# Performance work log

Hardware: AMD Instinct MI355X
Metric: run time of the kernel (lower is better)

## Reference

```python
import jax, jax.numpy as jnp
import numpy as np

B, S, DM, H, D = 4, 2048, 1024, 16, 64
CAP = 15.0
EPS = 1e-6


def setup_inputs() -> dict:
    key = jax.random.key(0)
    ks = jax.random.split(key, 5)
    return {
        "x": jax.random.normal(ks[0], (B, S, DM), jnp.float32),
        "hidden_state": jnp.zeros((B, H, D, D), jnp.float32),
        "w_qkv": jax.random.normal(ks[1], (3 * H * D, DM), jnp.float32) * 0.02,
        "w_gate": jax.random.normal(ks[2], (3 * H, DM), jnp.float32) * 0.02,
        "w_out": jax.random.normal(ks[3], (DM, H * D), jnp.float32) * 0.02,
        "ln_w": jnp.ones((DM,), jnp.float32),
    }


def reference(x, hidden_state, w_qkv, w_gate, w_out, ln_w):
    Bq, Sq, DMq = x.shape
    residual = x
    # RMSNorm (computed in float32, matching the torch module)
    xf = x.astype(jnp.float32)
    var = jnp.mean(xf * xf, axis=-1, keepdims=True)
    xn = ln_w * (xf * jax.lax.rsqrt(var + EPS)).astype(x.dtype)
    # Fused qkv projection: (B,S,3,H,D)
    qkv = jnp.einsum('bsd,od->bso', xn, w_qkv).reshape(Bq, Sq, 3, H, D)
    q, k, v = qkv[:, :, 0], qkv[:, :, 1], qkv[:, :, 2]
    # Gates: (B,S,3,H) -> soft cap -> sigmoid
    gates = jnp.einsum('bsd,od->bso', xn, w_gate).reshape(Bq, Sq, 3, H)
    gates = jax.nn.sigmoid(CAP * jnp.tanh(gates / CAP))
    ig, fg, og = gates[:, :, 0], gates[:, :, 1], gates[:, :, 2]

    def step(h, inp):
        q_t, k_t, v_t, i_t, f_t, o_t = inp  # q/k/v: (B,H,D); gates: (B,H)
        kv = jnp.einsum('bhd,bhe->bhde', k_t, v_t)
        h = f_t[..., None, None] * h + i_t[..., None, None] * kv
        out = o_t[..., None] * jnp.einsum('bhd,bhde->bhe', q_t, h)
        return h, out

    xs = (q.swapaxes(0, 1), k.swapaxes(0, 1), v.swapaxes(0, 1),
          ig.swapaxes(0, 1), fg.swapaxes(0, 1), og.swapaxes(0, 1))
    h_final, outs = jax.lax.scan(step, hidden_state, xs)  # outs: (S,B,H,D)
    output = outs.swapaxes(0, 1).reshape(Bq, Sq, H * D)
    y = residual + output @ w_out.T
    return y, h_final
```

## Files before the change

### kernel.cpp

```cpp
#include <hip/hip_runtime.h>
#include <hip/hip_bf16.h>
#include <math.h>
#include <stdint.h>

#define Bq 4
#define Sq 2048
#define DMq 1024
#define Hq 16
#define Dq 64
#define CAPf 15.0f
#define EPSf 1e-6f
#define Tc 64
#define Cc (Sq / Tc)
#define QKVW (3 * Hq * Dq)
#define NGATE (3 * Hq)
#define NMERGE (QKVW + NGATE)
#define NPAD 3200

typedef __attribute__((ext_vector_type(8))) short short8;
typedef __attribute__((ext_vector_type(4))) float f32x4;
typedef __hip_bfloat16 bf16;

__device__ __forceinline__ float b2f(bf16 v) { return __bfloat162float(v); }
__device__ __forceinline__ bf16  f2b(float v) { return __float2bfloat16(v); }
__device__ __forceinline__ uint16_t f2bu(float f) {
    bf16 h = __float2bfloat16(f); uint16_t u; __builtin_memcpy(&u, &h, 2); return u;
}
__device__ __forceinline__ float bu2f(uint16_t u) {
    uint32_t x = ((uint32_t)u) << 16; float f; __builtin_memcpy(&f, &x, 4); return f;
}
__device__ __forceinline__ float gate_act(float v) {
    float t = v * (1.0f / CAPf);
    float e2 = __expf(2.0f * t);
    float th = 1.0f - 2.0f / (e2 + 1.0f);
    return 1.0f / (1.0f + __expf(-CAPf * th));
}

__global__ void convert_all(const float* __restrict__ wqkv,
                            const float* __restrict__ wgate,
                            const float* __restrict__ wout,
                            bf16* __restrict__ wcomb, bf16* __restrict__ wob) {
    const int n1 = QKVW * DMq / 4;
    const int n2 = (NPAD - QKVW) * DMq / 4;
    const int ng = NGATE * DMq / 4;
    const int n3 = DMq * Hq * Dq / 4;
    int i = blockIdx.x * 256 + threadIdx.x;
    if (i < n1) {
        float4 v = ((const float4*)wqkv)[i];
        bf16 t[4] = {f2b(v.x), f2b(v.y), f2b(v.z), f2b(v.w)};
        ((uint2*)wcomb)[i] = *(uint2*)t;
    } else if (i < n1 + n2) {
        int j = i - n1;
        uint2 o = make_uint2(0u, 0u);
        if (j < ng) {
            float4 v = ((const float4*)wgate)[j];
            bf16 t[4] = {f2b(v.x), f2b(v.y), f2b(v.z), f2b(v.w)};
            o = *(uint2*)t;
        }
        ((uint2*)wcomb)[n1 + j] = o;
    } else if (i < n1 + n2 + n3) {
        int j = i - n1 - n2;
        float4 v = ((const float4*)wout)[j];
        bf16 t[4] = {f2b(v.x), f2b(v.y), f2b(v.z), f2b(v.w)};
        ((uint2*)wob)[j] = *(uint2*)t;
    }
}

__global__ void rmsnorm_kernel(const float* __restrict__ x,
                               const float* __restrict__ ln_w,
                               bf16* __restrict__ xn) {
    int row = blockIdx.x;
    const float4* xr = (const float4*)(x + (size_t)row * DMq);
    int tid = threadIdx.x;
    float4 v = xr[tid];
    float ss = v.x*v.x + v.y*v.y + v.z*v.z + v.w*v.w;
    #pragma unroll
    for (int off = 32; off > 0; off >>= 1) ss += __shfl_down(ss, off);
    __shared__ float red[4];
    int lane = tid & 63, wv = tid >> 6;
    if (lane == 0) red[wv] = ss;
    __syncthreads();
    float tot = red[0] + red[1] + red[2] + red[3];
    float rs = rsqrtf(tot * (1.0f / DMq) + EPSf);
    float4 w4 = ((const float4*)ln_w)[tid];
    bf16 t[4] = {f2b(v.x * rs * w4.x), f2b(v.y * rs * w4.y),
                 f2b(v.z * rs * w4.z), f2b(v.w * rs * w4.w)};
    *(uint2*)(xn + (size_t)row * DMq + tid * 4) = *(uint2*)t;
}

__device__ __forceinline__ int2 xcd_swizzle(int gx) {
    int wg = blockIdx.y * gx + blockIdx.x;
    int nwg = gx * gridDim.y;
    int cpx = nwg >> 3;
    int swz = (wg & 7) * cpx + (wg >> 3);
    return make_int2(swz % gx, swz / gx);
}

__global__ __launch_bounds__(256) void gemm_qkvgate(const bf16* __restrict__ A,
                                                    const bf16* __restrict__ Bw,
                                                    bf16* __restrict__ qkvb,
                                                    float* __restrict__ gates,
                                                    int M, int N, int K) {
    __shared__ bf16 As[128 * 64];
    __shared__ bf16 Bs[128 * 64];
    const int tid = threadIdx.x;
    const int w = tid >> 6;
    const int l = tid & 63;
    const int wr = (w >> 1) * 64;
    const int wc = (w & 1) * 64;
    int2 bxy = xcd_swizzle(gridDim.x);
    const int bm = bxy.y * 128;
    const int bn = bxy.x * 128;

    const int lrow = l >> 3;
    const int swzc = ((l & 7) ^ lrow) * 8;
    const int fl = l & 15;
    const int kb = l >> 4;
    const int rsw = l & 7;

    f32x4 acc[4][4];
    #pragma unroll
    for (int i = 0; i < 4; i++)
        #pragma unroll
        for (int j = 0; j < 4; j++) acc[i][j] = (f32x4){0.f, 0.f, 0.f, 0.f};

    for (int k0 = 0; k0 < K; k0 += 64) {
        __syncthreads();
        #pragma unroll
        for (int inst = 0; inst < 4; inst++) {
            int r0 = w * 32 + inst * 8;
            const bf16* gp = A + (size_t)(bm + r0 + lrow) * K + k0 + swzc;
            __builtin_amdgcn_global_load_lds(
                (const __attribute__((address_space(1))) uint32_t*)gp,
                (__attribute__((address_space(3))) uint32_t*)(As + r0 * 64),
                16, 0, 0);
        }
        #pragma unroll
        for (int inst = 0; inst < 4; inst++) {
            int r0 = w * 32 + inst * 8;
            if (bn + r0 < N) {
                const bf16* gp = Bw + (size_t)(bn + r0 + lrow) * K + k0 + swzc;
                __builtin_amdgcn_global_load_lds(
                    (const __attribute__((address_space(1))) uint32_t*)gp,
                    (__attribute__((address_space(3))) uint32_t*)(Bs + r0 * 64),
                    16, 0, 0);
            }
        }
        __syncthreads();
        #pragma unroll
        for (int kk2 = 0; kk2 < 2; kk2++) {
            const int koff = (((kk2 << 2) + kb) ^ rsw) * 8;
            short8 af[4], bfr[4];
            #pragma unroll
            for (int i = 0; i < 4; i++)
                af[i] = *(const short8*)(As + (wr + i * 16 + fl) * 64 + koff);
            #pragma unroll
            for (int j = 0; j < 4; j++)
                bfr[j] = *(const short8*)(Bs + (wc + j * 16 + fl) * 64 + koff);
            #pragma unroll
            for (int i = 0; i < 4; i++)
                #pragma unroll
                for (int j = 0; j < 4; j++)
                    acc[i][j] = __builtin_amdgcn_mfma_f32_16x16x32_bf16(
                        af[i], bfr[j], acc[i][j], 0, 0, 0);
        }
    }

    #pragma unroll
    for (int i = 0; i < 4; i++) {
        #pragma unroll
        for (int j = 0; j < 4; j++) {
            int col = bn + wc + j * 16 + fl;
            #pragma unroll
            for (int r = 0; r < 4; r++) {
                int row = bm + wr + i * 16 + kb * 4 + r;
                float v = acc[i][j][r];
                if (col < QKVW) {
                    qkvb[(size_t)row * QKVW + col] = f2b(v);
                } else if (col < NMERGE) {
                    gates[(size_t)row * NGATE + (col - QKVW)] = v;
                }
            }
        }
    }
}

__global__ __launch_bounds__(256) void gemm_out(const bf16* __restrict__ A,
                                                const bf16* __restrict__ Bw,
                                                const float* __restrict__ resid,
                                                float* __restrict__ C,
                                                int M, int N, int K) {
    __shared__ bf16 As[128 * 64];
    __shared__ bf16 Bs[128 * 64];
    const int tid = threadIdx.x;
    const int w = tid >> 6;
    const int l = tid & 63;
    const int wr = (w >> 1) * 64;
    const int wc = (w & 1) * 64;
    int2 bxy = xcd_swizzle(gridDim.x);
    const int bm = bxy.y * 128;
    const int bn = bxy.x * 128;

    const int lrow = l >> 3;
    const int swzc = ((l & 7) ^ lrow) * 8;
    const int fl = l & 15;
    const int kb = l >> 4;
    const int rsw = l & 7;

    f32x4 acc[4][4];
    #pragma unroll
    for (int i = 0; i < 4; i++)
        #pragma unroll
        for (int j = 0; j < 4; j++) acc[i][j] = (f32x4){0.f, 0.f, 0.f, 0.f};

    for (int k0 = 0; k0 < K; k0 += 64) {
        __syncthreads();
        #pragma unroll
        for (int inst = 0; inst < 4; inst++) {
            int r0 = w * 32 + inst * 8;
            const bf16* gp = A + (size_t)(bm + r0 + lrow) * K + k0 + swzc;
            __builtin_amdgcn_global_load_lds(
                (const __attribute__((address_space(1))) uint32_t*)gp,
                (__attribute__((address_space(3))) uint32_t*)(As + r0 * 64),
                16, 0, 0);
        }
        #pragma unroll
        for (int inst = 0; inst < 4; inst++) {
            int r0 = w * 32 + inst * 8;
            const bf16* gp = Bw + (size_t)(bn + r0 + lrow) * K + k0 + swzc;
            __builtin_amdgcn_global_load_lds(
                (const __attribute__((address_space(1))) uint32_t*)gp,
                (__attribute__((address_space(3))) uint32_t*)(Bs + r0 * 64),
                16, 0, 0);
        }
        __syncthreads();
        #pragma unroll
        for (int kk2 = 0; kk2 < 2; kk2++) {
            const int koff = (((kk2 << 2) + kb) ^ rsw) * 8;
            short8 af[4], bfr[4];
            #pragma unroll
            for (int i = 0; i < 4; i++)
                af[i] = *(const short8*)(As + (wr + i * 16 + fl) * 64 + koff);
            #pragma unroll
            for (int j = 0; j < 4; j++)
                bfr[j] = *(const short8*)(Bs + (wc + j * 16 + fl) * 64 + koff);
            #pragma unroll
            for (int i = 0; i < 4; i++)
                #pragma unroll
                for (int j = 0; j < 4; j++)
                    acc[i][j] = __builtin_amdgcn_mfma_f32_16x16x32_bf16(
                        af[i], bfr[j], acc[i][j], 0, 0, 0);
        }
    }

    #pragma unroll
    for (int i = 0; i < 4; i++) {
        #pragma unroll
        for (int j = 0; j < 4; j++) {
            int col = bn + wc + j * 16 + fl;
            #pragma unroll
            for (int r = 0; r < 4; r++) {
                int row = bm + wr + i * 16 + kb * 4 + r;
                size_t idx = (size_t)row * N + col;
                C[idx] = acc[i][j][r] + resid[idx];
            }
        }
    }
}

__global__ __launch_bounds__(64) void chunk_intra(const bf16* __restrict__ qkvb,
                                                  const float* __restrict__ gates,
                                                  bf16* __restrict__ attb,
                                                  bf16* __restrict__ LT,
                                                  float* __restrict__ oaArr,
                                                  float* __restrict__ Fch) {
    const int blk = blockIdx.x;
    const int c  = blk & (Cc - 1);
    const int bh = blk >> 5;
    const int b = bh >> 4, hh = bh & 15;
    const int l = threadIdx.x;
    const int s0 = c * Tc;

    __shared__ bf16 KTs[4096];
    __shared__ bf16 VTs[4096];
    __shared__ bf16 Ps[4096];
    __shared__ float rowS[64], pcolS[64], wstS[64];

    const float* gp = gates + (size_t)(b * Sq + s0 + l) * NGATE;
    float ig = gate_act(gp[hh]);
    float fg = gate_act(gp[Hq + hh]);
    float og = gate_act(gp[2 * Hq + hh]);
    float la = __logf(fg);
    #pragma unroll
    for (int off = 1; off < 64; off <<= 1) {
        float v = __shfl_up(la, off);
        if (l >= off) la += v;
    }
    float la63 = __shfl(la, 63);
    float li = __logf(ig);
    rowS[l]  = la + __logf(og);
    pcolS[l] = li - la;
    wstS[l]  = __expf(la63 - la + li);
    float oa = og * __expf(la);
    oaArr[(size_t)blk * 64 + l] = oa;
    if (l == 0) Fch[blk] = __expf(la63);
    __syncthreads();

    const int cg = l & 7, rp = l >> 3;
    const size_t rowBase = (size_t)(b * Sq + s0);
    const int kcol = (Hq + hh) * Dq, vcol = (2 * Hq + hh) * Dq;
    #pragma unroll
    for (int pass = 0; pass < 4; pass++) {
        int j0 = pass * 16 + rp * 2;
        const bf16* r0 = qkvb + (rowBase + j0) * QKVW;
        const bf16* r1 = qkvb + (rowBase + j0 + 1) * QKVW;
        short8 k0 = *(const short8*)(r0 + kcol + cg * 8);
        short8 k1 = *(const short8*)(r1 + kcol + cg * 8);
        short8 v0 = *(const short8*)(r0 + vcol + cg * 8);
        short8 v1 = *(const short8*)(r1 + vcol + cg * 8);
        float w0 = wstS[j0], w1 = wstS[j0 + 1];
        #pragma unroll
        for (int s = 0; s < 8; s++) {
            int cc = cg * 8 + s;
            int base = cc * 64 + ((((j0 >> 3) ^ (cc & 7) ^ (cc >> 3))) << 3) + (j0 & 7);
            uint32_t kp = (uint32_t)f2bu(bu2f((uint16_t)k0[s]) * w0)
                        | ((uint32_t)f2bu(bu2f((uint16_t)k1[s]) * w1) << 16);
            uint32_t vp = (uint32_t)(uint16_t)v0[s] | ((uint32_t)(uint16_t)v1[s] << 16);
            *(uint32_t*)&KTs[base] = kp;
            *(uint32_t*)&VTs[base] = vp;
        }
    }

    const int fl = l & 15, kb = l >> 4;
    const bf16* Qb = qkvb + rowBase * QKVW + hh * Dq;
    const bf16* Kb = qkvb + rowBase * QKVW + kcol;
    f32x4 accS[4][4];
    #pragma unroll
    for (int i = 0; i < 4; i++)
        #pragma unroll
        for (int j = 0; j < 4; j++) accS[i][j] = (f32x4){0.f, 0.f, 0.f, 0.f};
    #pragma unroll
    for (int ks = 0; ks < 2; ks++) {
        short8 qf[4], kf[4];
        #pragma unroll
        for (int i = 0; i < 4; i++)
            qf[i] = *(const short8*)(Qb + (size_t)(i * 16 + fl) * QKVW + ks * 32 + kb * 8);
        #pragma unroll
        for (int j = 0; j < 4; j++)
            kf[j] = *(const short8*)(Kb + (size_t)(j * 16 + fl) * QKVW + ks * 32 + kb * 8);
        #pragma unroll
        for (int i = 0; i < 4; i++)
            #pragma unroll
            for (int j = 0; j < 4; j++)
                accS[i][j] = __builtin_amdgcn_mfma_f32_16x16x32_bf16(qf[i], kf[j], accS[i][j], 0, 0, 0);
    }

    #pragma unroll
    for (int i = 0; i < 4; i++) {
        #pragma unroll
        for (int j = 0; j < 4; j++) {
            int jj = j * 16 + fl;
            float pc = pcolS[jj];
            #pragma unroll
            for (int r = 0; r < 4; r++) {
                int t = i * 16 + kb * 4 + r;
                float p = (jj <= t) ? __expf(rowS[t] + pc) * accS[i][j][r] : 0.f;
                int slot = (jj >> 3) ^ (t & 7) ^ (t >> 3);
                Ps[t * 64 + slot * 8 + (jj & 7)] = f2b(p);
            }
        }
    }
    __syncthreads();

    f32x4 accO[4][4], accL[4][4];
    #pragma unroll
    for (int i = 0; i < 4; i++)
        #pragma unroll
        for (int j = 0; j < 4; j++) {
            accO[i][j] = (f32x4){0.f, 0.f, 0.f, 0.f};
            accL[i][j] = (f32x4){0.f, 0.f, 0.f, 0.f};
        }
    #pragma unroll
    for (int ks = 0; ks < 2; ks++) {
        short8 pf[4], vt[4], kt[4];
        #pragma unroll
        for (int i = 0; i < 4; i++) {
            int row = i * 16 + fl;
            int koff = (((ks * 4 + kb) ^ (row & 7) ^ (row >> 3))) << 3;
            pf[i] = *(const short8*)(Ps  + row * 64 + koff);
            vt[i] = *(const short8*)(VTs + row * 64 + koff);
            kt[i] = *(const short8*)(KTs + row * 64 + koff);
        }
        #pragma unroll
        for (int i = 0; i < 4; i++)
            #pragma unroll
            for (int j = 0; j < 4; j++) {
                accO[i][j] = __builtin_amdgcn_mfma_f32_16x16x32_bf16(pf[i], vt[j], accO[i][j], 0, 0, 0);
                accL[i][j] = __builtin_amdgcn_mfma_f32_16x16x32_bf16(vt[i], kt[j], accL[i][j], 0, 0, 0);
            }
    }

    #pragma unroll
    for (int i = 0; i < 4; i++)
        #pragma unroll
        for (int j = 0; j < 4; j++)
            #pragma unroll
            for (int r = 0; r < 4; r++) {
                int rr = i * 16 + kb * 4 + r, cc2 = j * 16 + fl;
                attb[(rowBase + rr) * (Hq * Dq) + hh * Dq + cc2] = f2b(accO[i][j][r]);
                LT[(size_t)blk * 4096 + rr * 64 + cc2] = f2b(accL[i][j][r]);
            }
}

__global__ __launch_bounds__(256) void scan_pass2(bf16* __restrict__ LH,
                                                  const float* __restrict__ Fchunk,
                                                  const float* __restrict__ h0,
                                                  float* __restrict__ hfin) {
    int idx = blockIdx.x * 256 + threadIdx.x;
    int bh = idx >> 12;
    int ed = idx & 4095;
    int e = ed >> 6, d = ed & 63;
    float run = h0[(size_t)bh * 4096 + d * 64 + e];
    #pragma unroll
    for (int c = 0; c < Cc; c++) {
        float Fv = Fchunk[bh * Cc + c];
        size_t off = ((size_t)bh * Cc + c) * 4096 + ed;
        float Lv = b2f(LH[off]);
        LH[off] = f2b(run);
        run = Fv * run + Lv;
    }
    hfin[(size_t)bh * 4096 + d * 64 + e] = run;
}

__global__ __launch_bounds__(64) void chunk_cross(const bf16* __restrict__ qkvb,
                                                  const bf16* __restrict__ HT,
                                                  const float* __restrict__ oaArr,
                                                  bf16* __restrict__ attb) {
    const int blk = blockIdx.x;
    const int c = blk & (Cc - 1);
    const int bh = blk >> 5;
    const int b = bh >> 4, hh = bh & 15;
    const int l = threadIdx.x, fl = l & 15, kb = l >> 4;
    const size_t rowBase = (size_t)(b * Sq + c * Tc);
    __shared__ float oaS[64];
    oaS[l] = oaArr[(size_t)blk * 64 + l];
    __syncthreads();
    const bf16* Qb = qkvb + rowBase * QKVW + hh * Dq;
    const bf16* Hb = HT + (size_t)blk * 4096;
    f32x4 acc[4][4];
    #pragma unroll
    for (int i = 0; i < 4; i++)
        #pragma unroll
        for (int j = 0; j < 4; j++) acc[i][j] = (f32x4){0.f, 0.f, 0.f, 0.f};
    #pragma unroll
    for (int ks = 0; ks < 2; ks++) {
        short8 qf[4], hf[4];
        #pragma unroll
        for (int i = 0; i < 4; i++)
            qf[i] = *(const short8*)(Qb + (size_t)(i * 16 + fl) * QKVW + ks * 32 + kb * 8);
        #pragma unroll
        for (int j = 0; j < 4; j++)
            hf[j] = *(const short8*)(Hb + (j * 16 + fl) * 64 + ks * 32 + kb * 8);
        #pragma unroll
        for (int i = 0; i < 4; i++)
            #pragma unroll
            for (int j = 0; j < 4; j++)
                acc[i][j] = __builtin_amdgcn_mfma_f32_16x16x32_bf16(qf[i], hf[j], acc[i][j], 0, 0, 0);
    }
    #pragma unroll
    for (int i = 0; i < 4; i++)
        #pragma unroll
        for (int j = 0; j < 4; j++)
            #pragma unroll
            for (int r = 0; r < 4; r++) {
                int t = i * 16 + kb * 4 + r, e = j * 16 + fl;
                size_t idx = (rowBase + t) * (Hq * Dq) + hh * Dq + e;
                attb[idx] = f2b(b2f(attb[idx]) + oaS[t] * acc[i][j][r]);
            }
}

extern "C" void kernel_launch(void* const* d_in, const int* in_sizes, int n_in,
                              void* d_out, int out_size, void* d_ws, size_t ws_size,
                              hipStream_t stream) {
    const float* x      = (const float*)d_in[0];
    const float* h0     = (const float*)d_in[1];
    const float* w_qkv  = (const float*)d_in[2];
    const float* w_gate = (const float*)d_in[3];
    const float* w_out  = (const float*)d_in[4];
    const float* ln_w   = (const float*)d_in[5];

    const size_t MS = (size_t)Bq * Sq;
    const size_t BH = (size_t)Bq * Hq;

    float* p = (float*)d_ws;
    bf16*  xnb   = (bf16*)p;  p += MS * DMq / 2;
    bf16*  qkvb  = (bf16*)p;  p += MS * QKVW / 2;
    float* gates = p;         p += MS * NGATE;
    float* oaArr = p;         p += BH * Cc * Tc;
    float* Fch   = p;         p += BH * Cc;
    bf16*  LT    = (bf16*)p;  p += BH * Cc * Dq * Dq / 2;
    bf16*  wcomb = (bf16*)p;  p += (size_t)NPAD * DMq / 2;
    bf16*  wob   = (bf16*)p;  p += (size_t)DMq * Hq * Dq / 2;
    size_t need = (size_t)(p - (float*)d_ws) * sizeof(float);
    if (ws_size < need) return;
    bf16* attb = xnb;

    float* y    = (float*)d_out;
    float* hfin = y + MS * DMq;

    const int cvt_n = (QKVW * DMq + (NPAD - QKVW) * DMq + DMq * Hq * Dq) / 4;
    convert_all<<<dim3((cvt_n + 255) / 256), dim3(256), 0, stream>>>(
        w_qkv, w_gate, w_out, wcomb, wob);

    rmsnorm_kernel<<<dim3(MS), dim3(256), 0, stream>>>(x, ln_w, xnb);

    gemm_qkvgate<<<dim3(NPAD / 128, MS / 128), dim3(256), 0, stream>>>(
        xnb, wcomb, qkvb, gates, (int)MS, NPAD, DMq);

    chunk_intra<<<dim3(BH * Cc), dim3(64), 0, stream>>>(qkvb, gates, attb, LT, oaArr, Fch);
    scan_pass2<<<dim3(BH * 4096 / 256), dim3(256), 0, stream>>>(LT, Fch, h0, hfin);
    chunk_cross<<<dim3(BH * Cc), dim3(64), 0, stream>>>(qkvb, LT, oaArr, attb);

    gemm_out<<<dim3(DMq / 128, MS / 128), dim3(256), 0, stream>>>(
        attb, wob, x, y, (int)MS, DMq, Hq * Dq);
}
```

Baseline: 164.3 us.

## Merge rmsnorm into weight-convert launch and transpose gate storage

Folds the RMSNorm and the weight-conversion kernels into a single launch by dispatching on block index, which removes one kernel launch and its gap. Splits the QKV GEMM epilogue into a branch-free bf16 store path and a gate path. Gates are now stored transposed (gate-major, row-minor), so the chunk kernel reads them contiguously across lanes. Drops the N-bound guard on the B tile load, relying on the zero-padded NPAD weight buffer.

```diff
diff --git a/kernel.cpp b/kernel.cpp
--- a/kernel.cpp
+++ b/kernel.cpp
@@ -16,6 +16,7 @@
 #define NGATE (3 * Hq)
 #define NMERGE (QKVW + NGATE)
 #define NPAD 3200
+#define MSc (Bq * Sq)
 
 typedef __attribute__((ext_vector_type(8))) short short8;
 typedef __attribute__((ext_vector_type(4))) float f32x4;
@@ -36,15 +37,38 @@
     return 1.0f / (1.0f + __expf(-CAPf * th));
 }
 
-__global__ void convert_all(const float* __restrict__ wqkv,
+__global__ void prep_kernel(const float* __restrict__ x,
+                            const float* __restrict__ ln_w,
+                            const float* __restrict__ wqkv,
                             const float* __restrict__ wgate,
                             const float* __restrict__ wout,
+                            bf16* __restrict__ xn,
                             bf16* __restrict__ wcomb, bf16* __restrict__ wob) {
+    int tid = threadIdx.x;
+    if (blockIdx.x < MSc) {
+        int row = blockIdx.x;
+        const float4* xr = (const float4*)(x + (size_t)row * DMq);
+        float4 v = xr[tid];
+        float ss = v.x*v.x + v.y*v.y + v.z*v.z + v.w*v.w;
+        #pragma unroll
+        for (int off = 32; off > 0; off >>= 1) ss += __shfl_down(ss, off);
+        __shared__ float red[4];
+        int lane = tid & 63, wv = tid >> 6;
+        if (lane == 0) red[wv] = ss;
+        __syncthreads();
+        float tot = red[0] + red[1] + red[2] + red[3];
+        float rs = rsqrtf(tot * (1.0f / DMq) + EPSf);
+        float4 w4 = ((const float4*)ln_w)[tid];
+        bf16 t[4] = {f2b(v.x * rs * w4.x), f2b(v.y * rs * w4.y),
+                     f2b(v.z * rs * w4.z), f2b(v.w * rs * w4.w)};
+        *(uint2*)(xn + (size_t)row * DMq + tid * 4) = *(uint2*)t;
+        return;
+    }
     const int n1 = QKVW * DMq / 4;
     const int n2 = (NPAD - QKVW) * DMq / 4;
     const int ng = NGATE * DMq / 4;
     const int n3 = DMq * Hq * Dq / 4;
-    int i = blockIdx.x * 256 + threadIdx.x;
+    int i = (blockIdx.x - MSc) * 256 + tid;
     if (i < n1) {
         float4 v = ((const float4*)wqkv)[i];
         bf16 t[4] = {f2b(v.x), f2b(v.y), f2b(v.z), f2b(v.w)};
@@ -64,28 +88,6 @@
         bf16 t[4] = {f2b(v.x), f2b(v.y), f2b(v.z), f2b(v.w)};
         ((uint2*)wob)[j] = *(uint2*)t;
     }
-}
-
-__global__ void rmsnorm_kernel(const float* __restrict__ x,
-                               const float* __restrict__ ln_w,
-                               bf16* __restrict__ xn) {
-    int row = blockIdx.x;
-    const float4* xr = (const float4*)(x + (size_t)row * DMq);
-    int tid = threadIdx.x;
-    float4 v = xr[tid];
-    float ss = v.x*v.x + v.y*v.y + v.z*v.z + v.w*v.w;
-    #pragma unroll
-    for (int off = 32; off > 0; off >>= 1) ss += __shfl_down(ss, off);
-    __shared__ float red[4];
-    int lane = tid & 63, wv = tid >> 6;
-    if (lane == 0) red[wv] = ss;
-    __syncthreads();
-    float tot = red[0] + red[1] + red[2] + red[3];
-    float rs = rsqrtf(tot * (1.0f / DMq) + EPSf);
-    float4 w4 = ((const float4*)ln_w)[tid];
-    bf16 t[4] = {f2b(v.x * rs * w4.x), f2b(v.y * rs * w4.y),
-                 f2b(v.z * rs * w4.z), f2b(v.w * rs * w4.w)};
-    *(uint2*)(xn + (size_t)row * DMq + tid * 4) = *(uint2*)t;
 }
 
 __device__ __forceinline__ int2 xcd_swizzle(int gx) {
@@ -138,13 +140,11 @@
         #pragma unroll
         for (int inst = 0; inst < 4; inst++) {
             int r0 = w * 32 + inst * 8;
-            if (bn + r0 < N) {
-                const bf16* gp = Bw + (size_t)(bn + r0 + lrow) * K + k0 + swzc;
-                __builtin_amdgcn_global_load_lds(
-                    (const __attribute__((address_space(1))) uint32_t*)gp,
-                    (__attribute__((address_space(3))) uint32_t*)(Bs + r0 * 64),
-                    16, 0, 0);
-            }
+            const bf16* gp = Bw + (size_t)(bn + r0 + lrow) * K + k0 + swzc;
+            __builtin_amdgcn_global_load_lds(
+                (const __attribute__((address_space(1))) uint32_t*)gp,
+                (__attribute__((address_space(3))) uint32_t*)(Bs + r0 * 64),
+                16, 0, 0);
         }
         __syncthreads();
         #pragma unroll
@@ -166,19 +166,31 @@
         }
     }
 
-    #pragma unroll
-    for (int i = 0; i < 4; i++) {
-        #pragma unroll
-        for (int j = 0; j < 4; j++) {
-            int col = bn + wc + j * 16 + fl;
-            #pragma unroll
-            for (int r = 0; r < 4; r++) {
-                int row = bm + wr + i * 16 + kb * 4 + r;
-                float v = acc[i][j][r];
-                if (col < QKVW) {
-                    qkvb[(size_t)row * QKVW + col] = f2b(v);
-                } else if (col < NMERGE) {
-                    gates[(size_t)row * NGATE + (col - QKVW)] = v;
+    if (bn + 128 <= QKVW) {
+        #pragma unroll
+        for (int i = 0; i < 4; i++) {
+            #pragma unroll
+            for (int j = 0; j < 4; j++) {
+                int col = bn + wc + j * 16 + fl;
+                #pragma unroll
+                for (int r = 0; r < 4; r++) {
+                    int row = bm + wr + i * 16 + kb * 4 + r;
+                    qkvb[(size_t)row * QKVW + col] = f2b(acc[i][j][r]);
+                }
+            }
+        }
+    } else {
+        #pragma unroll
+        for (int i = 0; i < 4; i++) {
+            #pragma unroll
+            for (int j = 0; j < 4; j++) {
+                int g = bn + wc + j * 16 + fl - QKVW;
+                if (g < NGATE) {
+                    #pragma unroll
+                    for (int r = 0; r < 4; r++) {
+                        int row = bm + wr + i * 16 + kb * 4 + r;
+                        gates[(size_t)g * M + row] = acc[i][j][r];
+                    }
                 }
             }
         }
@@ -286,10 +298,10 @@
     __shared__ bf16 Ps[4096];
     __shared__ float rowS[64], pcolS[64], wstS[64];
 
-    const float* gp = gates + (size_t)(b * Sq + s0 + l) * NGATE;
-    float ig = gate_act(gp[hh]);
-    float fg = gate_act(gp[Hq + hh]);
-    float og = gate_act(gp[2 * Hq + hh]);
+    const int rix = b * Sq + s0 + l;
+    float ig = gate_act(gates[(size_t)(0 * Hq + hh) * MSc + rix]);
+    float fg = gate_act(gates[(size_t)(1 * Hq + hh) * MSc + rix]);
+    float og = gate_act(gates[(size_t)(2 * Hq + hh) * MSc + rix]);
     float la = __logf(fg);
     #pragma unroll
     for (int off = 1; off < 64; off <<= 1) {
@@ -509,10 +521,9 @@
     float* hfin = y + MS * DMq;
 
     const int cvt_n = (QKVW * DMq + (NPAD - QKVW) * DMq + DMq * Hq * Dq) / 4;
-    convert_all<<<dim3((cvt_n + 255) / 256), dim3(256), 0, stream>>>(
-        w_qkv, w_gate, w_out, wcomb, wob);
-
-    rmsnorm_kernel<<<dim3(MS), dim3(256), 0, stream>>>(x, ln_w, xnb);
+    const int cvt_blocks = (cvt_n + 255) / 256;
+    prep_kernel<<<dim3(MS + cvt_blocks), dim3(256), 0, stream>>>(
+        x, ln_w, w_qkv, w_gate, w_out, xnb, wcomb, wob);
 
     gemm_qkvgate<<<dim3(NPAD / 128, MS / 128), dim3(256), 0, stream>>>(
         xnb, wcomb, qkvb, gates, (int)MS, NPAD, DMq);
```

Result: slower. 173.2 us (+5.4%).
